# Performance work log

Measured on AMD Instinct MI355X. Metric: run time of the kernel, lower is better.

## Reference

```python
import jax, jax.numpy as jnp
import numpy as np

B, N, D, H, DK, DV, E = 32, 512, 128, 8, 16, 16, 128
MLP_H = 16


def _uniform(key, shape, fan):
    s = 1.0 / np.sqrt(fan)
    return jax.random.uniform(key, shape, jnp.float32, -s, s)


def setup_inputs() -> dict:
    key = jax.random.key(0)
    ks = jax.random.split(key, 13)
    q = jax.random.normal(ks[0], (B, N, D), jnp.float32)
    mask = jax.random.randint(ks[1], (B, N, N), 0, 2) > 0  # True = attention not allowed
    edge_matrix = jax.random.normal(ks[2], (B, N, N), jnp.float32)
    # per-head projection weights (init: uniform(-1/sqrt(last_dim), ...))
    W_query = _uniform(ks[3], (H, D, DK), DK)
    W_key = _uniform(ks[4], (H, D, DK), DK)
    W_val = _uniform(ks[5], (H, D, DV), DV)
    W_out = _uniform(ks[6], (H, DV, E), E)
    # edge MLP: 1 -> 16 -> 16 -> n_heads, ReLU between layers
    mlp_W1 = _uniform(ks[7], (1, MLP_H), 1)
    mlp_b1 = _uniform(ks[8], (MLP_H,), 1)
    mlp_W2 = _uniform(ks[9], (MLP_H, MLP_H), MLP_H)
    mlp_b2 = _uniform(ks[10], (MLP_H,), MLP_H)
    mlp_W3 = _uniform(ks[11], (MLP_H, H), MLP_H)
    mlp_b3 = _uniform(ks[12], (H,), MLP_H)
    return dict(q=q, mask=mask, edge_matrix=edge_matrix,
                W_query=W_query, W_key=W_key, W_val=W_val, W_out=W_out,
                mlp_W1=mlp_W1, mlp_b1=mlp_b1, mlp_W2=mlp_W2, mlp_b2=mlp_b2,
                mlp_W3=mlp_W3, mlp_b3=mlp_b3)


def reference(q, mask, edge_matrix, W_query, W_key, W_val, W_out,
              mlp_W1, mlp_b1, mlp_W2, mlp_b2, mlp_W3, mlp_b3):
    dk = W_query.shape[-1]
    norm = 1.0 / np.sqrt(dk)
    # per-head projections: [H,B,N,dk]
    Q = jnp.einsum('bni,hid->hbnd', q, W_query)
    K = jnp.einsum('bni,hid->hbnd', q, W_key)
    V = jnp.einsum('bni,hid->hbnd', q, W_val)
    # scaled QK^T: [H,B,N,N]
    comp = norm * jnp.einsum('hbqd,hbkd->hbqk', Q, K)
    # edge-bias MLP on each scalar edge weight: [B,N,N,1] -> [B,N,N,H]
    e = edge_matrix[..., None]
    h1 = jax.nn.relu(e @ mlp_W1 + mlp_b1)
    h2 = jax.nn.relu(h1 @ mlp_W2 + mlp_b2)
    bias = h2 @ mlp_W3 + mlp_b3
    comp = comp + jnp.transpose(bias, (3, 0, 1, 2))
    # masked softmax (mask True = disallowed)
    m = mask[None]  # broadcast over heads
    comp = jnp.where(m, -jnp.inf, comp)
    attn = jax.nn.softmax(comp, axis=-1)
    attn = jnp.where(m, 0.0, attn)
    heads = jnp.einsum('hbqk,hbkd->hbqd', attn, V)  # [H,B,N,dv]
    out = jnp.einsum('hbqd,hde->bqe', heads, W_out)  # [B,N,E]
    return out
```

## Files before the change

kernel.cpp:

```cpp
#include <hip/hip_runtime.h>
#include <hip/hip_bf16.h>
#include <float.h>

#define Bc 32
#define Nc 512
#define Dc 128
#define Hc 8
#define DKc 16
#define Ec 128
#define LOG2E 1.44269504088896340736f
#define SCLAMP 80.0f

typedef __attribute__((ext_vector_type(4))) short s16x4;
typedef __attribute__((ext_vector_type(8))) short s16x8;
typedef __attribute__((ext_vector_type(4))) float f32x4;

union BFU { __hip_bfloat16 b; short s; };
static __device__ inline short f2bf(float f) { BFU u; u.b = __float2bfloat16(f); return u.s; }
static __device__ inline s16x4 pack4(float a, float b, float c, float d) {
  s16x4 r; r[0] = f2bf(a); r[1] = f2bf(b); r[2] = f2bf(c); r[3] = f2bf(d); return r;
}

#if __has_builtin(__builtin_amdgcn_exp2f)
#define EXP2F(x) __builtin_amdgcn_exp2f(x)
#else
#define EXP2F(x) exp2f(x)
#endif

static __device__ inline f32x4 mfma16(s16x4 a, s16x4 b, f32x4 c) {
#if __has_builtin(__builtin_amdgcn_mfma_f32_16x16x16bf16_1k)
  return __builtin_amdgcn_mfma_f32_16x16x16bf16_1k(a, b, c, 0, 0, 0);
#else
  int lane = threadIdx.x & 63;
  int g = lane >> 4, base = lane & 15;
  int src0 = (base + 32 * g) & 63;
  int src1 = (base + 32 * g + 16) & 63;
  int ax = ((int*)&a)[0], ay = ((int*)&a)[1];
  int bx = ((int*)&b)[0], by = ((int*)&b)[1];
  int A0 = __shfl(ax, src0), A1 = __shfl(ay, src0);
  int A2 = __shfl(ax, src1), A3 = __shfl(ay, src1);
  int B0 = __shfl(bx, src0), B1 = __shfl(by, src0);
  int B2 = __shfl(bx, src1), B3 = __shfl(by, src1);
  if (g >= 2) { A0 = A1 = A2 = A3 = 0; B0 = B1 = B2 = B3 = 0; }
  s16x8 A8, B8;
  ((int*)&A8)[0] = A0; ((int*)&A8)[1] = A1; ((int*)&A8)[2] = A2; ((int*)&A8)[3] = A3;
  ((int*)&B8)[0] = B0; ((int*)&B8)[1] = B1; ((int*)&B8)[2] = B2; ((int*)&B8)[3] = B3;
  return __builtin_amdgcn_mfma_f32_16x16x32_bf16(A8, B8, c, 0, 0, 0);
#endif
}

__global__ __launch_bounds__(256) void prep_all(
    const float* __restrict__ Wq, const float* __restrict__ Wk, const float* __restrict__ Wv,
    const float* __restrict__ Wo,
    const unsigned char* __restrict__ m, int* __restrict__ flag,
    const float* __restrict__ mW1, const float* __restrict__ mb1,
    const float* __restrict__ mW2, const float* __restrict__ mb2,
    const float* __restrict__ mW3, const float* __restrict__ mb3,
    short* __restrict__ Wt, short* __restrict__ Wob, int* __restrict__ tabI)
{
  int blk = blockIdx.x;
  int t = threadIdx.x;

  if (blk == 256) {
    __shared__ int red[4];
    int any = 0;
    for (int u = t; u < 16384; u += 256)
      if ((u & 3) != 0 && m[u] != 0) any = 1;
    unsigned long long bal = __ballot(any != 0);
    if ((t & 63) == 0) red[t >> 6] = (bal != 0ULL) ? 1 : 0;
    __syncthreads();
    if (t == 0) *flag = red[0] | red[1] | red[2] | red[3];
    return;
  }

  if (blk >= 257) {
    __shared__ float wl[440];
    for (int u = t; u < 440; u += 256) {
      float v;
      if (u < 16) v = mW1[u];
      else if (u < 32)  v = mb1[u - 16];
      else if (u < 288) v = mW2[u - 32];
      else if (u < 304) v = mb2[u - 288];
      else if (u < 432) v = mW3[u - 304];
      else v = mb3[u - 432];
      wl[u] = v;
    }
    __syncthreads();
    int c = (blk - 257) * 256 + t;
    float mm = fmaf((float)c, 0.015625f, -7.9921875f);

    float pre[16];
    #pragma unroll
    for (int u = 0; u < 16; ++u) pre[u] = fmaf(mm, wl[u], wl[16 + u]);
    float a2[16], v2[16];
    #pragma unroll
    for (int v = 0; v < 16; ++v) { a2[v] = 0.f; v2[v] = wl[288 + v]; }
    #pragma unroll
    for (int u = 0; u < 16; ++u) {
      bool act = pre[u] > 0.f;
      float w1 = act ? wl[u] : 0.f;
      float pp = act ? pre[u] : 0.f;
      #pragma unroll
      for (int v = 0; v < 16; ++v) {
        float w2 = wl[32 + u * 16 + v];
        a2[v] = fmaf(w1, w2, a2[v]);
        v2[v] = fmaf(pp, w2, v2[v]);
      }
    }
    float ah[8], fh[8];
    #pragma unroll
    for (int h = 0; h < 8; ++h) { ah[h] = 0.f; fh[h] = wl[432 + h]; }
    #pragma unroll
    for (int v = 0; v < 16; ++v) {
      bool act = v2[v] > 0.f;
      float av = act ? a2[v] : 0.f;
      float vv = act ? v2[v] : 0.f;
      #pragma unroll
      for (int h = 0; h < 8; ++h) {
        float w3 = wl[304 + v * 8 + h];
        ah[h] = fmaf(av, w3, ah[h]);
        fh[h] = fmaf(vv, w3, fh[h]);
      }
    }
    #pragma unroll
    for (int h = 0; h < 8; ++h) {
      int ab = (int)(unsigned short)(f2bf(ah[h] * LOG2E));
      int fb = ((int)f2bf(fh[h] * LOG2E)) << 16;
      tabI[h * 1024 + c] = fb | ab;
    }
    return;
  }

  int o = blk * 256 + t;
  if (o < 49152) {
    int mat = o >> 14, r = o & 16383;
    int hk = r >> 7, d = r & 127;
    const float* src = (mat == 0) ? Wq : ((mat == 1) ? Wk : Wv);
    Wt[o] = f2bf(src[(hk >> 4) * 2048 + d * 16 + (hk & 15)]);
  } else {
    int o2 = o - 49152;
    int et = o2 >> 11, s = (o2 >> 8) & 7, lane = (o2 >> 2) & 63, i = o2 & 3;
    Wob[o2] = f2bf(Wo[(s * 16 + (lane >> 4) * 4 + i) * 128 + et * 16 + (lane & 15)]);
  }
}

__global__ __launch_bounds__(256, 4) void qkv4(
    const float* __restrict__ q, const short* __restrict__ Wt,
    short* __restrict__ Qb, short* __restrict__ Kb, short* __restrict__ Vt)
{
  __shared__ short qs[16][136];
  int blk = blockIdx.x;
  int b = blk >> 5;
  int rt = (blk & 31) << 4;
  int t = threadIdx.x;
  int wid = t >> 6, lane = t & 63;
  int lq = lane & 15, lg = lane >> 4;

  #pragma unroll
  for (int it = 0; it < 2; ++it) {
    int u = t + it * 256;
    int row = u >> 5, c4 = (u & 31) << 2;
    float4 v = *(const float4*)&q[((((b << 9) + rt + row) << 7)) + c4];
    *(s16x4*)&qs[row][c4] = pack4(v.x, v.y, v.z, v.w);
  }
  __syncthreads();

  s16x4 af[8];
  #pragma unroll
  for (int ks = 0; ks < 8; ++ks)
    af[ks] = *(const s16x4*)&qs[lq][ks * 16 + lg * 4];

  #pragma unroll 1
  for (int pj = 0; pj < 3; ++pj) {
    const short* Wm = Wt + pj * 16384;
    #pragma unroll
    for (int c2 = 0; c2 < 2; ++c2) {
      int ct = wid * 2 + c2;
      f32x4 acc = (f32x4)0.f;
      #pragma unroll
      for (int ks = 0; ks < 8; ++ks) {
        s16x4 bf = *(const s16x4*)&Wm[(ct * 16 + lq) * 128 + ks * 16 + lg * 4];
        acc = mfma16(af[ks], bf, acc);
      }
      if (pj == 0) {
        s16x4 pk = pack4(acc[0] * (0.25f * LOG2E), acc[1] * (0.25f * LOG2E),
                         acc[2] * (0.25f * LOG2E), acc[3] * (0.25f * LOG2E));
        #pragma unroll
        for (int r = 0; r < 4; ++r)
          Qb[(ct << 18) + (b << 13) + ((rt + lg * 4 + r) << 4) + lq] = pk[r];
      } else if (pj == 1) {
        s16x4 pk = pack4(acc[0], acc[1], acc[2], acc[3]);
        #pragma unroll
        for (int r = 0; r < 4; ++r)
          Kb[(ct << 18) + (b << 13) + ((rt + lg * 4 + r) << 4) + lq] = pk[r];
      } else {
        s16x4 pk = pack4(acc[0], acc[1], acc[2], acc[3]);
        *(s16x4*)&Vt[(ct << 18) + (((b << 4) + lq) << 9) + rt + lg * 4] = pk;
      }
    }
  }
}

__global__ __launch_bounds__(512) void attn13(
    const float* __restrict__ edge, const unsigned char* __restrict__ maskB,
    const int* __restrict__ flag,
    const short* __restrict__ Qb, const short* __restrict__ Kb, const short* __restrict__ Vt,
    const short* __restrict__ Wob,
    const int* __restrict__ tabI,
    float* __restrict__ out)
{
  __shared__ __align__(16) char smem[36864];

  int t = threadIdx.x;
  int wid = t >> 6, lane = t & 63;
  int lq = lane & 15, lg = lane >> 4;
  int b = blockIdx.x >> 5;
  int qt = (blockIdx.x & 31) << 4;
  int mflag = *flag;

  int* tabL = (int*)smem;
  s16x4* obfL = (s16x4*)smem;
  float* psL = (float*)(smem + 32768);

  for (int u = t; u < 2048; u += 512)
    ((int4*)smem)[u] = ((const int4*)tabI)[u];

  const short* Kl = Kb + (b << 13) + (lq << 4) + (lg << 2);
  const short* Vl = Vt + (((b << 4) + lq) << 9) + (lg << 2);
  const short* Ql = Qb + (b << 13) + ((qt + lq) << 4) + (lg << 2);
  unsigned mbase = (((b << 9) + qt + lq) << 9) + (lg << 2);

  s16x4 qf[8];
  #pragma unroll
  for (int h = 0; h < 8; ++h) qf[h] = *(const s16x4*)(Ql + (h << 18));

  f32x4 oacc[8];
  float psum[8];
  #pragma unroll
  for (int h = 0; h < 8; ++h) { oacc[h] = (f32x4)0.f; psum[h] = 0.f; }

  int jbA = wid << 4, jbB = (wid + 8) << 4;
  float4 evA = *(const float4*)&edge[mbase + jbA];
  float4 evB = *(const float4*)&edge[mbase + jbB];
  int4 mkA, mkB;
  if (mflag) {
    uchar4 ua = *(const uchar4*)&maskB[mbase + jbA];
    uchar4 ub = *(const uchar4*)&maskB[mbase + jbB];
    mkA.x = ua.x; mkA.y = ua.y; mkA.z = ua.z; mkA.w = ua.w;
    mkB.x = ub.x; mkB.y = ub.y; mkB.z = ub.z; mkB.w = ub.w;
  } else {
    mkA = *(const int4*)&((const int*)maskB)[mbase + jbA];
    mkB = *(const int4*)&((const int*)maskB)[mbase + jbB];
  }

  __syncthreads();

#define LOOKUP(ev, ix0, ix1, ix2, ix3, em0, em1, em2, em3) { \
    float fx0 = fminf(fmaxf(fmaf(ev.x, 64.f, 512.f), 0.f), 1023.f); \
    float fx1 = fminf(fmaxf(fmaf(ev.y, 64.f, 512.f), 0.f), 1023.f); \
    float fx2 = fminf(fmaxf(fmaf(ev.z, 64.f, 512.f), 0.f), 1023.f); \
    float fx3 = fminf(fmaxf(fmaf(ev.w, 64.f, 512.f), 0.f), 1023.f); \
    ix0 = (int)fx0; ix1 = (int)fx1; ix2 = (int)fx2; ix3 = (int)fx3; \
    em0 = ev.x - fmaf((float)ix0, 0.015625f, -7.9921875f); \
    em1 = ev.y - fmaf((float)ix1, 0.015625f, -7.9921875f); \
    em2 = ev.z - fmaf((float)ix2, 0.015625f, -7.9921875f); \
    em3 = ev.w - fmaf((float)ix3, 0.015625f, -7.9921875f); }

  #pragma unroll 1
  for (int cc = 0; cc < 2; ++cc) {
    jbA = (wid + 16 * cc) << 4;
    jbB = (wid + 16 * cc + 8) << 4;

    int ixA0, ixA1, ixA2, ixA3, ixB0, ixB1, ixB2, ixB3;
    float emA0, emA1, emA2, emA3, emB0, emB1, emB2, emB3;
    LOOKUP(evA, ixA0, ixA1, ixA2, ixA3, emA0, emA1, emA2, emA3)
    LOOKUP(evB, ixB0, ixB1, ixB2, ixB3, emB0, emB1, emB2, emB3)

    float4 evAn, evBn; int4 mkAn, mkBn;
    if (cc < 1) {
      int jbA2 = (wid + 16) << 4, jbB2 = (wid + 24) << 4;
      evAn = *(const float4*)&edge[mbase + jbA2];
      evBn = *(const float4*)&edge[mbase + jbB2];
      if (mflag) {
        uchar4 ua = *(const uchar4*)&maskB[mbase + jbA2];
        uchar4 ub = *(const uchar4*)&maskB[mbase + jbB2];
        mkAn.x = ua.x; mkAn.y = ua.y; mkAn.z = ua.z; mkAn.w = ua.w;
        mkBn.x = ub.x; mkBn.y = ub.y; mkBn.z = ub.z; mkBn.w = ub.w;
      } else {
        mkAn = *(const int4*)&((const int*)maskB)[mbase + jbA2];
        mkBn = *(const int4*)&((const int*)maskB)[mbase + jbB2];
      }
    } else { evAn = evA; evBn = evB; mkAn = mkA; mkBn = mkB; }

    #pragma unroll
    for (int h = 0; h < 8; ++h) {
      int a0 = tabL[(h << 10) + ixA0], a1 = tabL[(h << 10) + ixA1];
      int a2 = tabL[(h << 10) + ixA2], a3 = tabL[(h << 10) + ixA3];
      int b0 = tabL[(h << 10) + ixB0], b1 = tabL[(h << 10) + ixB1];
      int b2 = tabL[(h << 10) + ixB2], b3 = tabL[(h << 10) + ixB3];
      s16x4 kfA = *(const s16x4*)(Kl + (h << 18) + (jbA << 4));
      s16x4 kfB = *(const s16x4*)(Kl + (h << 18) + (jbB << 4));
      s16x4 vfA = *(const s16x4*)(Vl + (h << 18) + jbA);
      s16x4 vfB = *(const s16x4*)(Vl + (h << 18) + jbB);
      f32x4 scA, scB;
      scA[0] = fmaf(__int_as_float(a0 << 16), emA0, __int_as_float(a0 & 0xffff0000));
      scA[1] = fmaf(__int_as_float(a1 << 16), emA1, __int_as_float(a1 & 0xffff0000));
      scA[2] = fmaf(__int_as_float(a2 << 16), emA2, __int_as_float(a2 & 0xffff0000));
      scA[3] = fmaf(__int_as_float(a3 << 16), emA3, __int_as_float(a3 & 0xffff0000));
      scB[0] = fmaf(__int_as_float(b0 << 16), emB0, __int_as_float(b0 & 0xffff0000));
      scB[1] = fmaf(__int_as_float(b1 << 16), emB1, __int_as_float(b1 & 0xffff0000));
      scB[2] = fmaf(__int_as_float(b2 << 16), emB2, __int_as_float(b2 & 0xffff0000));
      scB[3] = fmaf(__int_as_float(b3 << 16), emB3, __int_as_float(b3 & 0xffff0000));
      scA = mfma16(kfA, qf[h], scA);
      scB = mfma16(kfB, qf[h], scB);
      float pA0 = mkA.x ? 0.f : EXP2F(fminf(scA[0], SCLAMP));
      float pA1 = mkA.y ? 0.f : EXP2F(fminf(scA[1], SCLAMP));
      float pA2 = mkA.z ? 0.f : EXP2F(fminf(scA[2], SCLAMP));
      float pA3 = mkA.w ? 0.f : EXP2F(fminf(scA[3], SCLAMP));
      float pB0 = mkB.x ? 0.f : EXP2F(fminf(scB[0], SCLAMP));
      float pB1 = mkB.y ? 0.f : EXP2F(fminf(scB[1], SCLAMP));
      float pB2 = mkB.z ? 0.f : EXP2F(fminf(scB[2], SCLAMP));
      float pB3 = mkB.w ? 0.f : EXP2F(fminf(scB[3], SCLAMP));
      psum[h] += ((pA0 + pA1) + (pA2 + pA3)) + ((pB0 + pB1) + (pB2 + pB3));
      s16x4 pfA = pack4(pA0, pA1, pA2, pA3);
      s16x4 pfB = pack4(pB0, pB1, pB2, pB3);
      oacc[h] = mfma16(vfA, pfA, oacc[h]);
      oacc[h] = mfma16(vfB, pfB, oacc[h]);
    }
    evA = evAn; evB = evBn; mkA = mkAn; mkB = mkBn;
  }
#undef LOOKUP

  #pragma unroll
  for (int h = 0; h < 8; ++h) {
    float s = psum[h];
    s += __shfl_xor(s, 16);
    s += __shfl_xor(s, 32);
    psum[h] = s;
  }
  if (lg == 0) {
    #pragma unroll
    for (int h = 0; h < 8; ++h) psL[(wid << 7) + (h << 4) + lq] = psum[h];
  }
  __syncthreads();

  #pragma unroll
  for (int h = 0; h < 8; ++h) {
    float tot = 0.f;
    #pragma unroll
    for (int w2 = 0; w2 < 8; ++w2) tot += psL[(w2 << 7) + (h << 4) + lq];
    float inv = (tot > 0.f) ? 1.f / tot : 0.f;
    obfL[((wid << 3) + h << 6) + lane] =
        pack4(oacc[h][0] * inv, oacc[h][1] * inv, oacc[h][2] * inv, oacc[h][3] * inv);
  }
  __syncthreads();

  {
    f32x4 d2a = (f32x4)0.f;
    #pragma unroll
    for (int s = 0; s < 8; ++s) {
      f32x4 fa = (f32x4)0.f;
      #pragma unroll
      for (int w2 = 0; w2 < 8; ++w2) {
        union { s16x4 v; int i[2]; } bb;
        bb.v = obfL[((w2 << 3) + s << 6) + lane];
        fa[0] += __int_as_float(bb.i[0] << 16);
        fa[1] += __int_as_float(bb.i[0] & 0xffff0000);
        fa[2] += __int_as_float(bb.i[1] << 16);
        fa[3] += __int_as_float(bb.i[1] & 0xffff0000);
      }
      s16x4 ob = pack4(fa[0], fa[1], fa[2], fa[3]);
      s16x4 wo = *(const s16x4*)&Wob[(((wid << 3) + s) << 8) + (lane << 2)];
      d2a = mfma16(wo, ob, d2a);
    }
    *(float4*)&out[((((b << 9) + qt + lq) << 7)) + (wid << 4) + (lg << 2)] =
        *(float4*)&d2a;
  }
}

extern "C" void kernel_launch(void* const* d_in, const int* in_sizes, int n_in,
                              void* d_out, int out_size, void* d_ws, size_t ws_size,
                              hipStream_t stream)
{
  const float* q    = (const float*)d_in[0];
  const unsigned char* mask = (const unsigned char*)d_in[1];
  const float* edge = (const float*)d_in[2];
  const float* Wq   = (const float*)d_in[3];
  const float* Wk   = (const float*)d_in[4];
  const float* Wv   = (const float*)d_in[5];
  const float* Wo   = (const float*)d_in[6];
  const float* mW1  = (const float*)d_in[7];
  const float* mb1  = (const float*)d_in[8];
  const float* mW2  = (const float*)d_in[9];
  const float* mb2  = (const float*)d_in[10];
  const float* mW3  = (const float*)d_in[11];
  const float* mb3  = (const float*)d_in[12];
  float* out = (float*)d_out;

  size_t per = (size_t)Hc * Bc * Nc * DKc;
  short* Wt  = (short*)d_ws;
  short* Wob = Wt + 49152;
  short* Qb  = Wob + 16384;
  short* Kb  = Qb + per;
  short* Vt  = Kb + per;
  int* tabI  = (int*)(Vt + per);
  int* flag  = tabI + 8192;

  prep_all<<<dim3(261), dim3(256), 0, stream>>>(Wq, Wk, Wv, Wo, mask, flag,
      mW1, mb1, mW2, mb2, mW3, mb3, Wt, Wob, tabI);
  qkv4<<<dim3(Bc * 32), dim3(256), 0, stream>>>(q, Wt, Qb, Kb, Vt);
  attn13<<<dim3(Bc * 32), dim3(512), 0, stream>>>(edge, mask, flag, Qb, Kb, Vt, Wob,
      tabI, out);
}
```

Before: 117.7 us.

## Prepack edge index, residual and mask into one word; pair heads in LUT

Adds blocks to the QKV projection kernel that convert each edge value and mask entry into a single 32-bit word holding the table index, the bf16 residual and a mask bit. The attention kernel then reads one packed stream instead of edge floats plus mask bytes, and skips the per-element index computation. The LDS table is interleaved so two heads' entries come from one 64-bit read, halving LDS lookups. The cost is an extra full B*N*N write and read pass through global memory in the projection kernel, plus bf16 rounding of the residual.

```diff
diff --git a/kernel.cpp b/kernel.cpp
--- a/kernel.cpp
+++ b/kernel.cpp
@@ -126,7 +126,7 @@
     for (int h = 0; h < 8; ++h) {
       int ab = (int)(unsigned short)(f2bf(ah[h] * LOG2E));
       int fb = ((int)f2bf(fh[h] * LOG2E)) << 16;
-      tabI[h * 1024 + c] = fb | ab;
+      tabI[(((h >> 1) << 10) + c) * 2 + (h & 1)] = fb | ab;
     }
     return;
   }
@@ -144,10 +144,38 @@
   }
 }
 
-__global__ __launch_bounds__(256, 4) void qkv4(
+static __device__ __forceinline__ unsigned packone(float e, int m) {
+  float fx = fminf(fmaxf(fmaf(e, 64.f, 512.f), 0.f), 1023.f);
+  int ix = (int)fx;
+  float em = e - fmaf((float)ix, 0.015625f, -7.9921875f);
+  return (m ? 0x80000000u : 0u) | ((unsigned)ix << 16) | (unsigned)(unsigned short)f2bf(em);
+}
+
+__global__ __launch_bounds__(256, 4) void qkv_pack(
     const float* __restrict__ q, const short* __restrict__ Wt,
-    short* __restrict__ Qb, short* __restrict__ Kb, short* __restrict__ Vt)
+    short* __restrict__ Qb, short* __restrict__ Kb, short* __restrict__ Vt,
+    const float* __restrict__ edge, const unsigned char* __restrict__ maskB,
+    const int* __restrict__ flag, unsigned* __restrict__ packed)
 {
+  if (blockIdx.x >= 1024) {
+    int idx = ((blockIdx.x - 1024) << 10) + ((int)threadIdx.x << 2);
+    float4 e4 = *(const float4*)&edge[idx];
+    int4 mk;
+    if (*flag) {
+      uchar4 u = *(const uchar4*)&maskB[idx];
+      mk.x = u.x; mk.y = u.y; mk.z = u.z; mk.w = u.w;
+    } else {
+      mk = *(const int4*)&((const int*)maskB)[idx];
+    }
+    uint4 o;
+    o.x = packone(e4.x, mk.x);
+    o.y = packone(e4.y, mk.y);
+    o.z = packone(e4.z, mk.z);
+    o.w = packone(e4.w, mk.w);
+    *(uint4*)&packed[idx] = o;
+    return;
+  }
+
   __shared__ short qs[16][136];
   int blk = blockIdx.x;
   int b = blk >> 5;
@@ -201,9 +229,8 @@
   }
 }
 
-__global__ __launch_bounds__(512) void attn13(
-    const float* __restrict__ edge, const unsigned char* __restrict__ maskB,
-    const int* __restrict__ flag,
+__global__ __launch_bounds__(512) void attn14(
+    const unsigned* __restrict__ packed,
     const short* __restrict__ Qb, const short* __restrict__ Kb, const short* __restrict__ Vt,
     const short* __restrict__ Wob,
     const int* __restrict__ tabI,
@@ -216,9 +243,8 @@
   int lq = lane & 15, lg = lane >> 4;
   int b = blockIdx.x >> 5;
   int qt = (blockIdx.x & 31) << 4;
-  int mflag = *flag;
-
-  int* tabL = (int*)smem;
+
+  const int2* tabP = (const int2*)smem;
   s16x4* obfL = (s16x4*)smem;
   float* psL = (float*)(smem + 32768);
 
@@ -239,97 +265,79 @@
   #pragma unroll
   for (int h = 0; h < 8; ++h) { oacc[h] = (f32x4)0.f; psum[h] = 0.f; }
 
-  int jbA = wid << 4, jbB = (wid + 8) << 4;
-  float4 evA = *(const float4*)&edge[mbase + jbA];
-  float4 evB = *(const float4*)&edge[mbase + jbB];
-  int4 mkA, mkB;
-  if (mflag) {
-    uchar4 ua = *(const uchar4*)&maskB[mbase + jbA];
-    uchar4 ub = *(const uchar4*)&maskB[mbase + jbB];
-    mkA.x = ua.x; mkA.y = ua.y; mkA.z = ua.z; mkA.w = ua.w;
-    mkB.x = ub.x; mkB.y = ub.y; mkB.z = ub.z; mkB.w = ub.w;
-  } else {
-    mkA = *(const int4*)&((const int*)maskB)[mbase + jbA];
-    mkB = *(const int4*)&((const int*)maskB)[mbase + jbB];
-  }
+  uint4 puA = *(const uint4*)&packed[mbase + (wid << 4)];
+  uint4 puB = *(const uint4*)&packed[mbase + ((wid + 8) << 4)];
 
   __syncthreads();
-
-#define LOOKUP(ev, ix0, ix1, ix2, ix3, em0, em1, em2, em3) { \
-    float fx0 = fminf(fmaxf(fmaf(ev.x, 64.f, 512.f), 0.f), 1023.f); \
-    float fx1 = fminf(fmaxf(fmaf(ev.y, 64.f, 512.f), 0.f), 1023.f); \
-    float fx2 = fminf(fmaxf(fmaf(ev.z, 64.f, 512.f), 0.f), 1023.f); \
-    float fx3 = fminf(fmaxf(fmaf(ev.w, 64.f, 512.f), 0.f), 1023.f); \
-    ix0 = (int)fx0; ix1 = (int)fx1; ix2 = (int)fx2; ix3 = (int)fx3; \
-    em0 = ev.x - fmaf((float)ix0, 0.015625f, -7.9921875f); \
-    em1 = ev.y - fmaf((float)ix1, 0.015625f, -7.9921875f); \
-    em2 = ev.z - fmaf((float)ix2, 0.015625f, -7.9921875f); \
-    em3 = ev.w - fmaf((float)ix3, 0.015625f, -7.9921875f); }
 
   #pragma unroll 1
   for (int cc = 0; cc < 2; ++cc) {
-    jbA = (wid + 16 * cc) << 4;
-    jbB = (wid + 16 * cc + 8) << 4;
-
-    int ixA0, ixA1, ixA2, ixA3, ixB0, ixB1, ixB2, ixB3;
-    float emA0, emA1, emA2, emA3, emB0, emB1, emB2, emB3;
-    LOOKUP(evA, ixA0, ixA1, ixA2, ixA3, emA0, emA1, emA2, emA3)
-    LOOKUP(evB, ixB0, ixB1, ixB2, ixB3, emB0, emB1, emB2, emB3)
-
-    float4 evAn, evBn; int4 mkAn, mkBn;
+    int jbA = (wid + 16 * cc) << 4;
+    int jbB = (wid + 16 * cc + 8) << 4;
+
+    float emA[4], emB[4]; int ixA[4], ixB[4], mkA[4], mkB[4];
+    #pragma unroll
+    for (int r = 0; r < 4; ++r) {
+      unsigned uA = ((const unsigned*)&puA)[r];
+      unsigned uB = ((const unsigned*)&puB)[r];
+      emA[r] = __int_as_float((int)(uA << 16));
+      ixA[r] = (int)((uA >> 16) & 0x3FFu);
+      mkA[r] = (int)uA >> 31;
+      emB[r] = __int_as_float((int)(uB << 16));
+      ixB[r] = (int)((uB >> 16) & 0x3FFu);
+      mkB[r] = (int)uB >> 31;
+    }
+
+    uint4 puAn, puBn;
     if (cc < 1) {
-      int jbA2 = (wid + 16) << 4, jbB2 = (wid + 24) << 4;
-      evAn = *(const float4*)&edge[mbase + jbA2];
-      evBn = *(const float4*)&edge[mbase + jbB2];
-      if (mflag) {
-        uchar4 ua = *(const uchar4*)&maskB[mbase + jbA2];
-        uchar4 ub = *(const uchar4*)&maskB[mbase + jbB2];
-        mkAn.x = ua.x; mkAn.y = ua.y; mkAn.z = ua.z; mkAn.w = ua.w;
-        mkBn.x = ub.x; mkBn.y = ub.y; mkBn.z = ub.z; mkBn.w = ub.w;
-      } else {
-        mkAn = *(const int4*)&((const int*)maskB)[mbase + jbA2];
-        mkBn = *(const int4*)&((const int*)maskB)[mbase + jbB2];
-      }
-    } else { evAn = evA; evBn = evB; mkAn = mkA; mkBn = mkB; }
-
-    #pragma unroll
-    for (int h = 0; h < 8; ++h) {
-      int a0 = tabL[(h << 10) + ixA0], a1 = tabL[(h << 10) + ixA1];
-      int a2 = tabL[(h << 10) + ixA2], a3 = tabL[(h << 10) + ixA3];
-      int b0 = tabL[(h << 10) + ixB0], b1 = tabL[(h << 10) + ixB1];
-      int b2 = tabL[(h << 10) + ixB2], b3 = tabL[(h << 10) + ixB3];
-      s16x4 kfA = *(const s16x4*)(Kl + (h << 18) + (jbA << 4));
-      s16x4 kfB = *(const s16x4*)(Kl + (h << 18) + (jbB << 4));
-      s16x4 vfA = *(const s16x4*)(Vl + (h << 18) + jbA);
-      s16x4 vfB = *(const s16x4*)(Vl + (h << 18) + jbB);
-      f32x4 scA, scB;
-      scA[0] = fmaf(__int_as_float(a0 << 16), emA0, __int_as_float(a0 & 0xffff0000));
-      scA[1] = fmaf(__int_as_float(a1 << 16), emA1, __int_as_float(a1 & 0xffff0000));
-      scA[2] = fmaf(__int_as_float(a2 << 16), emA2, __int_as_float(a2 & 0xffff0000));
-      scA[3] = fmaf(__int_as_float(a3 << 16), emA3, __int_as_float(a3 & 0xffff0000));
-      scB[0] = fmaf(__int_as_float(b0 << 16), emB0, __int_as_float(b0 & 0xffff0000));
-      scB[1] = fmaf(__int_as_float(b1 << 16), emB1, __int_as_float(b1 & 0xffff0000));
-      scB[2] = fmaf(__int_as_float(b2 << 16), emB2, __int_as_float(b2 & 0xffff0000));
-      scB[3] = fmaf(__int_as_float(b3 << 16), emB3, __int_as_float(b3 & 0xffff0000));
-      scA = mfma16(kfA, qf[h], scA);
-      scB = mfma16(kfB, qf[h], scB);
-      float pA0 = mkA.x ? 0.f : EXP2F(fminf(scA[0], SCLAMP));
-      float pA1 = mkA.y ? 0.f : EXP2F(fminf(scA[1], SCLAMP));
-      float pA2 = mkA.z ? 0.f : EXP2F(fminf(scA[2], SCLAMP));
-      float pA3 = mkA.w ? 0.f : EXP2F(fminf(scA[3], SCLAMP));
-      float pB0 = mkB.x ? 0.f : EXP2F(fminf(scB[0], SCLAMP));
-      float pB1 = mkB.y ? 0.f : EXP2F(fminf(scB[1], SCLAMP));
-      float pB2 = mkB.z ? 0.f : EXP2F(fminf(scB[2], SCLAMP));
-      float pB3 = mkB.w ? 0.f : EXP2F(fminf(scB[3], SCLAMP));
-      psum[h] += ((pA0 + pA1) + (pA2 + pA3)) + ((pB0 + pB1) + (pB2 + pB3));
-      s16x4 pfA = pack4(pA0, pA1, pA2, pA3);
-      s16x4 pfB = pack4(pB0, pB1, pB2, pB3);
-      oacc[h] = mfma16(vfA, pfA, oacc[h]);
-      oacc[h] = mfma16(vfB, pfB, oacc[h]);
-    }
-    evA = evAn; evB = evBn; mkA = mkAn; mkB = mkBn;
-  }
-#undef LOOKUP
+      puAn = *(const uint4*)&packed[mbase + ((wid + 16) << 4)];
+      puBn = *(const uint4*)&packed[mbase + ((wid + 24) << 4)];
+    } else { puAn = puA; puBn = puB; }
+
+    #pragma unroll
+    for (int hp = 0; hp < 4; ++hp) {
+      const int2* tp = tabP + (hp << 10);
+      int2 cA0 = tp[ixA[0]], cA1 = tp[ixA[1]], cA2 = tp[ixA[2]], cA3 = tp[ixA[3]];
+      int2 cB0 = tp[ixB[0]], cB1 = tp[ixB[1]], cB2 = tp[ixB[2]], cB3 = tp[ixB[3]];
+      #pragma unroll
+      for (int e = 0; e < 2; ++e) {
+        int h = hp * 2 + e;
+        int a0 = e ? cA0.y : cA0.x, a1 = e ? cA1.y : cA1.x;
+        int a2 = e ? cA2.y : cA2.x, a3 = e ? cA3.y : cA3.x;
+        int b0 = e ? cB0.y : cB0.x, b1 = e ? cB1.y : cB1.x;
+        int b2 = e ? cB2.y : cB2.x, b3 = e ? cB3.y : cB3.x;
+        s16x4 kfA = *(const s16x4*)(Kl + (h << 18) + (jbA << 4));
+        s16x4 kfB = *(const s16x4*)(Kl + (h << 18) + (jbB << 4));
+        s16x4 vfA = *(const s16x4*)(Vl + (h << 18) + jbA);
+        s16x4 vfB = *(const s16x4*)(Vl + (h << 18) + jbB);
+        f32x4 scA, scB;
+        scA[0] = fmaf(__int_as_float(a0 << 16), emA[0], __int_as_float(a0 & 0xffff0000));
+        scA[1] = fmaf(__int_as_float(a1 << 16), emA[1], __int_as_float(a1 & 0xffff0000));
+        scA[2] = fmaf(__int_as_float(a2 << 16), emA[2], __int_as_float(a2 & 0xffff0000));
+        scA[3] = fmaf(__int_as_float(a3 << 16), emA[3], __int_as_float(a3 & 0xffff0000));
+        scB[0] = fmaf(__int_as_float(b0 << 16), emB[0], __int_as_float(b0 & 0xffff0000));
+        scB[1] = fmaf(__int_as_float(b1 << 16), emB[1], __int_as_float(b1 & 0xffff0000));
+        scB[2] = fmaf(__int_as_float(b2 << 16), emB[2], __int_as_float(b2 & 0xffff0000));
+        scB[3] = fmaf(__int_as_float(b3 << 16), emB[3], __int_as_float(b3 & 0xffff0000));
+        scA = mfma16(kfA, qf[h], scA);
+        scB = mfma16(kfB, qf[h], scB);
+        float pA0 = mkA[0] ? 0.f : EXP2F(fminf(scA[0], SCLAMP));
+        float pA1 = mkA[1] ? 0.f : EXP2F(fminf(scA[1], SCLAMP));
+        float pA2 = mkA[2] ? 0.f : EXP2F(fminf(scA[2], SCLAMP));
+        float pA3 = mkA[3] ? 0.f : EXP2F(fminf(scA[3], SCLAMP));
+        float pB0 = mkB[0] ? 0.f : EXP2F(fminf(scB[0], SCLAMP));
+        float pB1 = mkB[1] ? 0.f : EXP2F(fminf(scB[1], SCLAMP));
+        float pB2 = mkB[2] ? 0.f : EXP2F(fminf(scB[2], SCLAMP));
+        float pB3 = mkB[3] ? 0.f : EXP2F(fminf(scB[3], SCLAMP));
+        psum[h] += ((pA0 + pA1) + (pA2 + pA3)) + ((pB0 + pB1) + (pB2 + pB3));
+        s16x4 pfA = pack4(pA0, pA1, pA2, pA3);
+        s16x4 pfB = pack4(pB0, pB1, pB2, pB3);
+        oacc[h] = mfma16(vfA, pfA, oacc[h]);
+        oacc[h] = mfma16(vfB, pfB, oacc[h]);
+      }
+    }
+    puA = puAn; puB = puBn;
+  }
 
   #pragma unroll
   for (int h = 0; h < 8; ++h) {
@@ -405,10 +413,11 @@
   short* Vt  = Kb + per;
   int* tabI  = (int*)(Vt + per);
   int* flag  = tabI + 8192;
+  unsigned* packed = (unsigned*)(flag + 4);
 
   prep_all<<<dim3(261), dim3(256), 0, stream>>>(Wq, Wk, Wv, Wo, mask, flag,
       mW1, mb1, mW2, mb2, mW3, mb3, Wt, Wob, tabI);
-  qkv4<<<dim3(Bc * 32), dim3(256), 0, stream>>>(q, Wt, Qb, Kb, Vt);
-  attn13<<<dim3(Bc * 32), dim3(512), 0, stream>>>(edge, mask, flag, Qb, Kb, Vt, Wob,
-      tabI, out);
-}
+  qkv_pack<<<dim3(1024 + 8192), dim3(256), 0, stream>>>(q, Wt, Qb, Kb, Vt,
+      edge, mask, flag, packed);
+  attn14<<<dim3(Bc * 32), dim3(512), 0, stream>>>(packed, Qb, Kb, Vt, Wob, tabI, out);
+}
```

Result: slower. 166.0 us (+41.0%).
